# Optimization experiments

Measured on AMD Instinct MI355X. Metric: run time of the kernel, lower is better.

Reference implementation:

```python
import jax, jax.numpy as jnp
import numpy as np

N = 100000
E = 1_600_000
IN = 128
HID = 32
HEADS = 4
OUT = 2
NEG_SLOPE = 0.2  # PyG GATv2Conv default negative_slope


def setup_inputs() -> dict:
    key = jax.random.key(0)
    ks = jax.random.split(key, 18)
    g = lambda k, shape, fan: jax.random.normal(k, shape, dtype=jnp.float32) / np.sqrt(fan)
    return {
        "x": jax.random.normal(ks[0], (N, IN), dtype=jnp.float32),
        "edge_index": jax.random.randint(ks[1], (2, E), 0, N, dtype=jnp.int32),
        # conv1: GATv2Conv(IN, HID, heads=HEADS)
        "W1l": g(ks[2], (IN, HEADS * HID), IN),
        "b1l": jnp.zeros((HEADS * HID,), jnp.float32),
        "W1r": g(ks[3], (IN, HEADS * HID), IN),
        "b1r": jnp.zeros((HEADS * HID,), jnp.float32),
        "att1": g(ks[4], (HEADS, HID), HID),
        "bias1": jnp.zeros((HEADS * HID,), jnp.float32),
        # conv2: GATv2Conv(HEADS*HID, HID, heads=1)
        "W2l": g(ks[5], (HEADS * HID, HID), HEADS * HID),
        "b2l": jnp.zeros((HID,), jnp.float32),
        "W2r": g(ks[6], (HEADS * HID, HID), HEADS * HID),
        "b2r": jnp.zeros((HID,), jnp.float32),
        "att2": g(ks[7], (1, HID), HID),
        "bias2": jnp.zeros((HID,), jnp.float32),
        # final linear
        "Wlin": g(ks[8], (HID, OUT), HID),
        "blin": jnp.zeros((OUT,), jnp.float32),
    }


def _gatv2(x, src, dst, Wl, bl, Wr, br, att, bias, heads, ch):
    n = x.shape[0]
    xl = (x @ Wl + bl).reshape(n, heads, ch)  # source transform
    xr = (x @ Wr + br).reshape(n, heads, ch)  # target transform
    # GATv2 edge score: a^T LeakyReLU(xl_j + xr_i)
    e = jax.nn.leaky_relu(xl[src] + xr[dst], NEG_SLOPE)      # [E, H, C]
    score = jnp.einsum('ehc,hc->eh', e, att)                  # [E, H]
    # segment softmax over edges sharing a destination node
    m = jax.ops.segment_max(score, dst, num_segments=n)
    ex = jnp.exp(score - m[dst])
    denom = jax.ops.segment_sum(ex, dst, num_segments=n)
    alpha = ex / denom[dst]                                   # [E, H]
    out = jax.ops.segment_sum(alpha[..., None] * xl[src], dst, num_segments=n)
    return out.reshape(n, heads * ch) + bias


def reference(x, edge_index, W1l, b1l, W1r, b1r, att1, bias1,
              W2l, b2l, W2r, b2r, att2, bias2, Wlin, blin):
    # add self-loops (PyG GATv2Conv default add_self_loops=True)
    loop = jnp.arange(N, dtype=edge_index.dtype)
    src = jnp.concatenate([edge_index[0], loop])
    dst = jnp.concatenate([edge_index[1], loop])

    h = _gatv2(x, src, dst, W1l, b1l, W1r, b1r, att1, bias1, HEADS, HID)
    h = jax.nn.elu(h)
    # dropout is inactive in eval mode
    h = _gatv2(h, src, dst, W2l, b2l, W2r, b2r, att2, bias2, 1, HID)
    h = jax.nn.elu(h)
    return h @ Wlin + blin  # [N, OUT]
```

## Files before the change

kernel.cpp:

```cpp
#include <hip/hip_runtime.h>
#include <hip/hip_fp16.h>
#include <math.h>

#define N_NODES 100000
#define E_EDGES 1600000
#define ETOT (E_EDGES + N_NODES)
#define NEG 0.2f
#define NB 782
#define BCAP 2560
#define CHUNK 8192
#define NCHB ((ETOT + CHUNK - 1) / CHUNK)

typedef _Float16 half8 __attribute__((ext_vector_type(8)));
typedef _Float16 half4v __attribute__((ext_vector_type(4)));
typedef _Float16 half2v __attribute__((ext_vector_type(2)));
typedef float floatx4 __attribute__((ext_vector_type(4)));

union H8 {
  half8 v;
  _Float16 e[8];
};

__device__ __forceinline__ float elu(float v) { return v > 0.f ? v : (__expf(v) - 1.f); }

__device__ __forceinline__ float score8(half8 a, half8 r, half8 av) {
  half8 t = a + r;
  t = __builtin_elementwise_max(t, t * (_Float16)NEG);
  half8 s8 = t * av;
  half4v s4 = __builtin_shufflevector(s8, s8, 0, 1, 2, 3) +
              __builtin_shufflevector(s8, s8, 4, 5, 6, 7);
  half2v s2 = __builtin_shufflevector(s4, s4, 0, 1) +
              __builtin_shufflevector(s4, s4, 2, 3);
  return (float)s2[0] + (float)s2[1];
}

__global__ __launch_bounds__(256) void bin_kernel(const int* __restrict__ ei,
                                                  unsigned* __restrict__ cursor,
                                                  unsigned* __restrict__ bins) {
  __shared__ unsigned cnt[NB];
  __shared__ unsigned base[NB];
  int t = threadIdx.x;
  for (int b = t; b < NB; b += 256) cnt[b] = 0;
  __syncthreads();
  int e0 = blockIdx.x * CHUNK;
#pragma unroll
  for (int i = 0; i < CHUNK / 256; i++) {
    int e = e0 + i * 256 + t;
    if (e < ETOT) {
      int dst = (e < E_EDGES) ? ei[E_EDGES + e] : (e - E_EDGES);
      atomicAdd(&cnt[dst >> 7], 1u);
    }
  }
  __syncthreads();
  for (int b = t; b < NB; b += 256) {
    unsigned c = cnt[b];
    base[b] = c ? atomicAdd(&cursor[b], c) : 0u;
    cnt[b] = 0;
  }
  __syncthreads();
#pragma unroll
  for (int i = 0; i < CHUNK / 256; i++) {
    int e = e0 + i * 256 + t;
    if (e < ETOT) {
      int src, dst;
      if (e < E_EDGES) { src = ei[e]; dst = ei[E_EDGES + e]; }
      else { src = e - E_EDGES; dst = src; }
      int b = dst >> 7;
      unsigned off = atomicAdd(&cnt[b], 1u);
      bins[(size_t)b * BCAP + base[b] + off] =
          ((unsigned)(dst & 127) << 17) | (unsigned)src;
    }
  }
}

__global__ __launch_bounds__(1024) void scan_buckets(const unsigned* __restrict__ cursor,
                                                     unsigned* __restrict__ bucket_base,
                                                     unsigned* __restrict__ rowptr) {
  __shared__ unsigned s[1024];
  int t = threadIdx.x;
  unsigned v = (t < NB) ? cursor[t] : 0u;
  s[t] = v;
  __syncthreads();
  for (int off = 1; off < 1024; off <<= 1) {
    unsigned a = (t >= off) ? s[t - off] : 0u;
    __syncthreads();
    s[t] += a;
    __syncthreads();
  }
  if (t < NB) bucket_base[t] = s[t] - v;
  if (t == 0) { bucket_base[NB] = ETOT; rowptr[N_NODES] = ETOT; }
}

__global__ __launch_bounds__(256) void scatter2_kernel(const unsigned* __restrict__ bins,
                                                       const unsigned* __restrict__ cursor,
                                                       const unsigned* __restrict__ bucket_base,
                                                       unsigned* __restrict__ rowptr,
                                                       int* __restrict__ csr_src) {
  __shared__ unsigned cnt[128];
  __shared__ unsigned pref[128];
  int b = blockIdx.x, t = threadIdx.x;
  unsigned cntb = cursor[b];
  unsigned bbase = bucket_base[b];
  const unsigned* bp = bins + (size_t)b * BCAP;
  if (t < 128) cnt[t] = 0;
  __syncthreads();
  for (unsigned i = t; i < cntb; i += 256) atomicAdd(&cnt[bp[i] >> 17], 1u);
  __syncthreads();
  if (t < 128) pref[t] = cnt[t];
  __syncthreads();
  for (int off = 1; off < 128; off <<= 1) {
    unsigned a = (t >= off && t < 128) ? pref[t - off] : 0u;
    __syncthreads();
    if (t < 128) pref[t] += a;
    __syncthreads();
  }
  if (t < 128) {
    unsigned excl = pref[t] - cnt[t];
    pref[t] = excl;
    int n = (b << 7) + t;
    if (n < N_NODES) rowptr[n] = bbase + excl;
    cnt[t] = 0;
  }
  __syncthreads();
  for (unsigned i = t; i < cntb; i += 256) {
    unsigned en = bp[i];
    int j = (int)(en >> 17);
    unsigned off = atomicAdd(&cnt[j], 1u);
    csr_src[bbase + pref[j] + off] = (int)(en & 0x1FFFFu);
  }
}

__global__ __launch_bounds__(256) void pack_w_kernel(
    const float* __restrict__ W1l, const float* __restrict__ W1r,
    const float* __restrict__ b1l, const float* __restrict__ b1r,
    const float* __restrict__ W2l, const float* __restrict__ W2r,
    const float* __restrict__ b2l, const float* __restrict__ b2r,
    const float* __restrict__ att1, const float* __restrict__ att2,
    _Float16* __restrict__ Bperm, _Float16* __restrict__ B2perm,
    float* __restrict__ biascat, float* __restrict__ bias2cat,
    _Float16* __restrict__ att1h, _Float16* __restrict__ att2h) {
  int gt = blockIdx.x * 256 + threadIdx.x;
  int gstr = gridDim.x * 256;
  for (int e = gt; e < 4096; e += gstr) {
    int nt = e >> 8, kt = (e >> 6) & 3, lane = e & 63;
    int n = nt * 16 + (lane & 15);
    int kb = kt * 32 + (lane >> 4) * 8;
#pragma unroll
    for (int j = 0; j < 8; j++) {
      int k = kb + j;
      float val = (n < 128) ? W1l[k * 128 + n] : W1r[k * 128 + (n - 128)];
      Bperm[(size_t)e * 8 + j] = (_Float16)val;
    }
  }
  for (int e = gt; e < 1024; e += gstr) {
    int nt = e >> 8, kt = (e >> 6) & 3, lane = e & 63;
    int n = nt * 16 + (lane & 15);
    int kb = kt * 32 + (lane >> 4) * 8;
#pragma unroll
    for (int j = 0; j < 8; j++) {
      int k = kb + j;
      float val = (n < 32) ? W2l[k * 32 + n] : W2r[k * 32 + (n - 32)];
      B2perm[(size_t)e * 8 + j] = (_Float16)val;
    }
  }
  if (blockIdx.x == 0) {
    int t = threadIdx.x;
    biascat[t] = (t < 128) ? b1l[t] : b1r[t - 128];
    if (t < 64) bias2cat[t] = (t < 32) ? b2l[t] : b2r[t - 32];
    if (t < 128) att1h[t] = (_Float16)att1[t];
    if (t < 32) att2h[t] = (_Float16)att2[t];
  }
}

__global__ __launch_bounds__(256) void gemm1_mfma(
    const float* __restrict__ x, const _Float16* __restrict__ Bperm,
    const float* __restrict__ biascat,
    __half* __restrict__ xlh, __half* __restrict__ xrh) {
  __shared__ __align__(16) char smem[64 * 256];
  int t = threadIdx.x;
  int base = blockIdx.x * 64;
  {
    int row = t >> 2, c4 = t & 3;
    int grow = base + row;
    const float* gp = x + (size_t)grow * 128 + c4 * 32;
#pragma unroll
    for (int j = 0; j < 4; j++) {
      half8 v = {};
      if (grow < N_NODES) {
        float4 f0 = *(const float4*)(gp + j * 8);
        float4 f1 = *(const float4*)(gp + j * 8 + 4);
        v[0] = (_Float16)f0.x; v[1] = (_Float16)f0.y;
        v[2] = (_Float16)f0.z; v[3] = (_Float16)f0.w;
        v[4] = (_Float16)f1.x; v[5] = (_Float16)f1.y;
        v[6] = (_Float16)f1.z; v[7] = (_Float16)f1.w;
      }
      int off = row * 256 + ((((c4 * 4 + j) * 16)) ^ ((row & 7) << 4));
      *(half8*)(smem + off) = v;
    }
  }
  int wid = t >> 6, lane = t & 63;
  half8 bf[4][4];
#pragma unroll
  for (int ntl = 0; ntl < 4; ntl++)
#pragma unroll
    for (int kt = 0; kt < 4; kt++) {
      int f = (wid * 4 + ntl) * 4 + kt;
      bf[ntl][kt] = *(const half8*)(Bperm + ((size_t)f * 64 + lane) * 8);
    }
  floatx4 acc[4][4] = {};
  __syncthreads();
#pragma unroll
  for (int kt = 0; kt < 4; kt++) {
    half8 a[4];
#pragma unroll
    for (int mt = 0; mt < 4; mt++) {
      int row = mt * 16 + (lane & 15);
      int kchunk = kt * 4 + (lane >> 4);
      int off = row * 256 + ((kchunk * 16) ^ ((row & 7) << 4));
      a[mt] = *(const half8*)(smem + off);
    }
#pragma unroll
    for (int mt = 0; mt < 4; mt++)
#pragma unroll
      for (int ntl = 0; ntl < 4; ntl++)
        acc[mt][ntl] = __builtin_amdgcn_mfma_f32_16x16x32_f16(a[mt], bf[ntl][kt],
                                                              acc[mt][ntl], 0, 0, 0);
  }
#pragma unroll
  for (int mt = 0; mt < 4; mt++) {
#pragma unroll
    for (int i = 0; i < 4; i++) {
      int row = base + mt * 16 + (lane >> 4) * 4 + i;
      if (row >= N_NODES) continue;
#pragma unroll
      for (int ntl = 0; ntl < 4; ntl++) {
        int col = wid * 64 + ntl * 16 + (lane & 15);
        float v = acc[mt][ntl][i] + biascat[col];
        if (col < 128) xlh[(size_t)row * 128 + col] = __float2half_rn(v);
        else xrh[(size_t)row * 128 + (col - 128)] = __float2half_rn(v);
      }
    }
  }
}

__global__ __launch_bounds__(256) void gemm2_mfma(
    const __half* __restrict__ h1h, const _Float16* __restrict__ B2perm,
    const float* __restrict__ bias2cat,
    __half* __restrict__ xl2h, __half* __restrict__ xr2h) {
  __shared__ __align__(16) char smem[64 * 256];
  int t = threadIdx.x;
  int base = blockIdx.x * 64;
  {
    int row = t >> 2, c4 = t & 3;
    int grow = base + row;
    const char* gp = (const char*)(h1h + (size_t)grow * 128 + c4 * 32);
#pragma unroll
    for (int j = 0; j < 4; j++) {
      half8 v = {};
      if (grow < N_NODES) v = *(const half8*)(gp + j * 16);
      int off = row * 256 + ((((c4 * 4 + j) * 16)) ^ ((row & 7) << 4));
      *(half8*)(smem + off) = v;
    }
  }
  int wid = t >> 6, lane = t & 63;
  half8 bf[4];
#pragma unroll
  for (int kt = 0; kt < 4; kt++) {
    int f = wid * 4 + kt;
    bf[kt] = *(const half8*)(B2perm + ((size_t)f * 64 + lane) * 8);
  }
  floatx4 acc[4] = {};
  __syncthreads();
#pragma unroll
  for (int kt = 0; kt < 4; kt++) {
    half8 a[4];
#pragma unroll
    for (int mt = 0; mt < 4; mt++) {
      int row = mt * 16 + (lane & 15);
      int kchunk = kt * 4 + (lane >> 4);
      int off = row * 256 + ((kchunk * 16) ^ ((row & 7) << 4));
      a[mt] = *(const half8*)(smem + off);
    }
#pragma unroll
    for (int mt = 0; mt < 4; mt++)
      acc[mt] = __builtin_amdgcn_mfma_f32_16x16x32_f16(a[mt], bf[kt], acc[mt], 0, 0, 0);
  }
  int col = wid * 16 + (lane & 15);
  float bv = bias2cat[col];
#pragma unroll
  for (int mt = 0; mt < 4; mt++) {
#pragma unroll
    for (int i = 0; i < 4; i++) {
      int row = base + mt * 16 + (lane >> 4) * 4 + i;
      if (row >= N_NODES) continue;
      float v = acc[mt][i] + bv;
      if (col < 32) xl2h[(size_t)row * 32 + col] = __float2half_rn(v);
      else xr2h[(size_t)row * 32 + (col - 32)] = __float2half_rn(v);
    }
  }
}

__global__ __launch_bounds__(256) void l1_gather_kernel(
    const __half* __restrict__ xlh, const __half* __restrict__ xrh,
    const int* __restrict__ csr_src, const unsigned* __restrict__ rowptr,
    const _Float16* __restrict__ att1h, const float* __restrict__ bias,
    __half* __restrict__ h1h) {
  int wid = threadIdx.x >> 6;
  int lane = threadIdx.x & 63;
  int n = blockIdx.x * 4 + wid;
  if (n >= N_NODES) return;
  int g = lane >> 4;
  int q = lane & 15;
  int c0 = q * 8;
  half8 rv = *(const half8*)(xrh + (size_t)n * 128 + c0);
  half8 av = *(const half8*)(att1h + c0);
  unsigned beg = rowptr[n], end = rowptr[n + 1];
  int nit = (int)(end - beg + 3) >> 2;
  float d = 0.f;
  float acc[8] = {0.f};
  for (int i = 0; i < nit; i++) {
    unsigned e = beg + i * 4 + g;
    bool valid = e < end;
    int s = csr_src[valid ? e : (end - 1)];
    H8 a;
    a.v = *(const half8*)(xlh + (size_t)s * 128 + c0);
    float v = score8(a.v, rv, av);
    v += __shfl_xor(v, 1);
    v += __shfl_xor(v, 2);
    float p = valid ? __expf(v) : 0.f;
    d += p;
#pragma unroll
    for (int j = 0; j < 8; j++) acc[j] = fmaf(p, (float)a.e[j], acc[j]);
  }
#pragma unroll
  for (int msk = 16; msk <= 32; msk <<= 1) {
    d += __shfl_xor(d, msk);
#pragma unroll
    for (int j = 0; j < 8; j++) acc[j] += __shfl_xor(acc[j], msk);
  }
  if (g == 0) {
    float inv = 1.f / d;
    H8 res;
#pragma unroll
    for (int j = 0; j < 8; j++)
      res.e[j] = (_Float16)elu(acc[j] * inv + bias[c0 + j]);
    *(half8*)(h1h + (size_t)n * 128 + c0) = res.v;
  }
}

__global__ __launch_bounds__(256) void l2_gather_kernel(
    const __half* __restrict__ xl2h, const __half* __restrict__ xr2h,
    const int* __restrict__ csr_src, const unsigned* __restrict__ rowptr,
    const _Float16* __restrict__ att2h, const float* __restrict__ bias,
    const float* __restrict__ Wlin, const float* __restrict__ blin,
    float* __restrict__ out) {
  int wid = threadIdx.x >> 6;
  int lane = threadIdx.x & 63;
  int n = blockIdx.x * 4 + wid;
  if (n >= N_NODES) return;
  int g = lane >> 2;
  int q = lane & 3;
  int c0 = q * 8;
  half8 rv = *(const half8*)(xr2h + (size_t)n * 32 + c0);
  half8 av = *(const half8*)(att2h + c0);
  unsigned beg = rowptr[n], end = rowptr[n + 1];
  int nit = (int)(end - beg + 15) >> 4;
  float d = 0.f;
  float acc[8] = {0.f};
  for (int i = 0; i < nit; i++) {
    unsigned e = beg + i * 16 + g;
    bool valid = e < end;
    int s = csr_src[valid ? e : (end - 1)];
    H8 a;
    a.v = *(const half8*)(xl2h + (size_t)s * 32 + c0);
    float v = score8(a.v, rv, av);
    v += __shfl_xor(v, 1);
    v += __shfl_xor(v, 2);
    float p = valid ? __expf(v) : 0.f;
    d += p;
#pragma unroll
    for (int j = 0; j < 8; j++) acc[j] = fmaf(p, (float)a.e[j], acc[j]);
  }
#pragma unroll
  for (int msk = 4; msk <= 32; msk <<= 1) {
    d += __shfl_xor(d, msk);
#pragma unroll
    for (int j = 0; j < 8; j++) acc[j] += __shfl_xor(acc[j], msk);
  }
  float inv = 1.f / d;
  float o0 = 0.f, o1 = 0.f;
#pragma unroll
  for (int j = 0; j < 8; j++) {
    float v = elu(acc[j] * inv + bias[c0 + j]);
    o0 = fmaf(v, Wlin[(c0 + j) * 2 + 0], o0);
    o1 = fmaf(v, Wlin[(c0 + j) * 2 + 1], o1);
  }
  o0 += __shfl_xor(o0, 1); o1 += __shfl_xor(o1, 1);
  o0 += __shfl_xor(o0, 2); o1 += __shfl_xor(o1, 2);
  if (lane == 0) {
    out[(size_t)n * 2 + 0] = o0 + blin[0];
    out[(size_t)n * 2 + 1] = o1 + blin[1];
  }
}

extern "C" void kernel_launch(void* const* d_in, const int* in_sizes, int n_in,
                              void* d_out, int out_size, void* d_ws, size_t ws_size,
                              hipStream_t stream) {
  const float* x     = (const float*)d_in[0];
  const int*   ei    = (const int*)d_in[1];
  const float* W1l   = (const float*)d_in[2];
  const float* b1l   = (const float*)d_in[3];
  const float* W1r   = (const float*)d_in[4];
  const float* b1r   = (const float*)d_in[5];
  const float* att1  = (const float*)d_in[6];
  const float* bias1 = (const float*)d_in[7];
  const float* W2l   = (const float*)d_in[8];
  const float* b2l   = (const float*)d_in[9];
  const float* W2r   = (const float*)d_in[10];
  const float* b2r   = (const float*)d_in[11];
  const float* att2  = (const float*)d_in[12];
  const float* bias2 = (const float*)d_in[13];
  const float* Wlin  = (const float*)d_in[14];
  const float* blin  = (const float*)d_in[15];
  float* out = (float*)d_out;

  __half* xl1h  = (__half*)d_ws;
  __half* xr1h  = xl1h + (size_t)N_NODES * 128;
  __half* h1h   = xr1h + (size_t)N_NODES * 128;
  __half* xl2h  = h1h + (size_t)N_NODES * 128;
  __half* xr2h  = xl2h + (size_t)N_NODES * 32;
  _Float16* Bperm  = (_Float16*)(xr2h + (size_t)N_NODES * 32);
  _Float16* B2perm = Bperm + 32768;
  _Float16* att1h  = B2perm + 8192;
  _Float16* att2h  = att1h + 128;
  float* biascat   = (float*)(att2h + 32);
  float* bias2cat  = biascat + 256;
  int* csr_src     = (int*)(bias2cat + 64);
  unsigned* rowptr = (unsigned*)(csr_src + (size_t)ETOT);
  unsigned* cursor = rowptr + (N_NODES + 1);
  unsigned* bucket_base = cursor + NB;
  unsigned* bins   = bucket_base + NB + 1;

  pack_w_kernel<<<20, 256, 0, stream>>>(W1l, W1r, b1l, b1r, W2l, W2r, b2l, b2r,
                                        att1, att2, Bperm, B2perm, biascat, bias2cat,
                                        att1h, att2h);

  (void)hipMemsetAsync(cursor, 0, (size_t)NB * sizeof(unsigned), stream);
  bin_kernel<<<NCHB, 256, 0, stream>>>(ei, cursor, bins);
  scan_buckets<<<1, 1024, 0, stream>>>(cursor, bucket_base, rowptr);
  scatter2_kernel<<<NB, 256, 0, stream>>>(bins, cursor, bucket_base, rowptr, csr_src);

  gemm1_mfma<<<(N_NODES + 63) / 64, 256, 0, stream>>>(x, Bperm, biascat, xl1h, xr1h);
  l1_gather_kernel<<<(N_NODES + 3) / 4, 256, 0, stream>>>(
      (const __half*)xl1h, (const __half*)xr1h, csr_src, rowptr, att1h, bias1, h1h);

  gemm2_mfma<<<(N_NODES + 63) / 64, 256, 0, stream>>>(h1h, B2perm, bias2cat, xl2h, xr2h);
  l2_gather_kernel<<<(N_NODES + 3) / 4, 256, 0, stream>>>(
      xl2h, xr2h, csr_src, rowptr, att2h, bias2, Wlin, blin, out);
}
```

Measured before the change: 266.6 us.

## Fuse independent kernels by block range and accumulate gathers in half precision

```diff
diff --git a/kernel.cpp b/kernel.cpp
--- a/kernel.cpp
+++ b/kernel.cpp
@@ -10,15 +10,17 @@
 #define BCAP 2560
 #define CHUNK 8192
 #define NCHB ((ETOT + CHUNK - 1) / CHUNK)
+#define GEMM1_BLOCKS ((N_NODES + 63) / 64)
 
 typedef _Float16 half8 __attribute__((ext_vector_type(8)));
 typedef _Float16 half4v __attribute__((ext_vector_type(4)));
 typedef _Float16 half2v __attribute__((ext_vector_type(2)));
 typedef float floatx4 __attribute__((ext_vector_type(4)));
 
-union H8 {
+union H8I {
   half8 v;
   _Float16 e[8];
+  int i[4];
 };
 
 __device__ __forceinline__ float elu(float v) { return v > 0.f ? v : (__expf(v) - 1.f); }
@@ -34,41 +36,85 @@
   return (float)s2[0] + (float)s2[1];
 }
 
-__global__ __launch_bounds__(256) void bin_kernel(const int* __restrict__ ei,
-                                                  unsigned* __restrict__ cursor,
-                                                  unsigned* __restrict__ bins) {
-  __shared__ unsigned cnt[NB];
-  __shared__ unsigned base[NB];
+__global__ __launch_bounds__(256) void fusedA_kernel(
+    const int* __restrict__ ei, unsigned* __restrict__ cursor,
+    unsigned* __restrict__ bins,
+    const float* __restrict__ W1l, const float* __restrict__ W1r,
+    const float* __restrict__ b1l, const float* __restrict__ b1r,
+    const float* __restrict__ W2l, const float* __restrict__ W2r,
+    const float* __restrict__ b2l, const float* __restrict__ b2r,
+    const float* __restrict__ att1, const float* __restrict__ att2,
+    _Float16* __restrict__ Bperm, _Float16* __restrict__ B2perm,
+    float* __restrict__ biascat, float* __restrict__ bias2cat,
+    _Float16* __restrict__ att1h, _Float16* __restrict__ att2h) {
   int t = threadIdx.x;
-  for (int b = t; b < NB; b += 256) cnt[b] = 0;
-  __syncthreads();
-  int e0 = blockIdx.x * CHUNK;
-#pragma unroll
-  for (int i = 0; i < CHUNK / 256; i++) {
-    int e = e0 + i * 256 + t;
-    if (e < ETOT) {
-      int dst = (e < E_EDGES) ? ei[E_EDGES + e] : (e - E_EDGES);
-      atomicAdd(&cnt[dst >> 7], 1u);
-    }
-  }
-  __syncthreads();
-  for (int b = t; b < NB; b += 256) {
-    unsigned c = cnt[b];
-    base[b] = c ? atomicAdd(&cursor[b], c) : 0u;
-    cnt[b] = 0;
-  }
-  __syncthreads();
-#pragma unroll
-  for (int i = 0; i < CHUNK / 256; i++) {
-    int e = e0 + i * 256 + t;
-    if (e < ETOT) {
-      int src, dst;
-      if (e < E_EDGES) { src = ei[e]; dst = ei[E_EDGES + e]; }
-      else { src = e - E_EDGES; dst = src; }
-      int b = dst >> 7;
-      unsigned off = atomicAdd(&cnt[b], 1u);
-      bins[(size_t)b * BCAP + base[b] + off] =
-          ((unsigned)(dst & 127) << 17) | (unsigned)src;
+  if (blockIdx.x < NCHB) {
+    __shared__ unsigned cnt[NB];
+    __shared__ unsigned base[NB];
+    for (int b = t; b < NB; b += 256) cnt[b] = 0;
+    __syncthreads();
+    int e0 = blockIdx.x * CHUNK;
+    int dstr[CHUNK / 256];
+#pragma unroll
+    for (int i = 0; i < CHUNK / 256; i++) {
+      int e = e0 + i * 256 + t;
+      int dst = 0;
+      if (e < ETOT) {
+        dst = (e < E_EDGES) ? ei[E_EDGES + e] : (e - E_EDGES);
+        atomicAdd(&cnt[dst >> 7], 1u);
+      }
+      dstr[i] = dst;
+    }
+    __syncthreads();
+    for (int b = t; b < NB; b += 256) {
+      unsigned c = cnt[b];
+      base[b] = c ? atomicAdd(&cursor[b], c) : 0u;
+      cnt[b] = 0;
+    }
+    __syncthreads();
+#pragma unroll
+    for (int i = 0; i < CHUNK / 256; i++) {
+      int e = e0 + i * 256 + t;
+      if (e < ETOT) {
+        int dst = dstr[i];
+        int src = (e < E_EDGES) ? ei[e] : dst;
+        int b = dst >> 7;
+        unsigned off = atomicAdd(&cnt[b], 1u);
+        bins[(size_t)b * BCAP + base[b] + off] =
+            ((unsigned)(dst & 127) << 17) | (unsigned)src;
+      }
+    }
+  } else {
+    int pb = blockIdx.x - NCHB;
+    int gt = pb * 256 + t;
+    int gstr = 20 * 256;
+    for (int e = gt; e < 4096; e += gstr) {
+      int nt = e >> 8, kt = (e >> 6) & 3, lane = e & 63;
+      int n = nt * 16 + (lane & 15);
+      int kb = kt * 32 + (lane >> 4) * 8;
+#pragma unroll
+      for (int j = 0; j < 8; j++) {
+        int k = kb + j;
+        float val = (n < 128) ? W1l[k * 128 + n] : W1r[k * 128 + (n - 128)];
+        Bperm[(size_t)e * 8 + j] = (_Float16)val;
+      }
+    }
+    for (int e = gt; e < 1024; e += gstr) {
+      int nt = e >> 8, kt = (e >> 6) & 3, lane = e & 63;
+      int n = nt * 16 + (lane & 15);
+      int kb = kt * 32 + (lane >> 4) * 8;
+#pragma unroll
+      for (int j = 0; j < 8; j++) {
+        int k = kb + j;
+        float val = (n < 32) ? W2l[k * 32 + n] : W2r[k * 32 + (n - 32)];
+        B2perm[(size_t)e * 8 + j] = (_Float16)val;
+      }
+    }
+    if (pb == 0) {
+      biascat[t] = (t < 128) ? b1l[t] : b1r[t - 128];
+      if (t < 64) bias2cat[t] = (t < 32) ? b2l[t] : b2r[t - 32];
+      if (t < 128) att1h[t] = (_Float16)att1[t];
+      if (t < 32) att2h[t] = (_Float16)att2[t];
     }
   }
 }
@@ -91,153 +137,110 @@
   if (t == 0) { bucket_base[NB] = ETOT; rowptr[N_NODES] = ETOT; }
 }
 
-__global__ __launch_bounds__(256) void scatter2_kernel(const unsigned* __restrict__ bins,
-                                                       const unsigned* __restrict__ cursor,
-                                                       const unsigned* __restrict__ bucket_base,
-                                                       unsigned* __restrict__ rowptr,
-                                                       int* __restrict__ csr_src) {
-  __shared__ unsigned cnt[128];
-  __shared__ unsigned pref[128];
-  int b = blockIdx.x, t = threadIdx.x;
-  unsigned cntb = cursor[b];
-  unsigned bbase = bucket_base[b];
-  const unsigned* bp = bins + (size_t)b * BCAP;
-  if (t < 128) cnt[t] = 0;
-  __syncthreads();
-  for (unsigned i = t; i < cntb; i += 256) atomicAdd(&cnt[bp[i] >> 17], 1u);
-  __syncthreads();
-  if (t < 128) pref[t] = cnt[t];
-  __syncthreads();
-  for (int off = 1; off < 128; off <<= 1) {
-    unsigned a = (t >= off && t < 128) ? pref[t - off] : 0u;
-    __syncthreads();
-    if (t < 128) pref[t] += a;
-    __syncthreads();
-  }
-  if (t < 128) {
-    unsigned excl = pref[t] - cnt[t];
-    pref[t] = excl;
-    int n = (b << 7) + t;
-    if (n < N_NODES) rowptr[n] = bbase + excl;
-    cnt[t] = 0;
-  }
-  __syncthreads();
-  for (unsigned i = t; i < cntb; i += 256) {
-    unsigned en = bp[i];
-    int j = (int)(en >> 17);
-    unsigned off = atomicAdd(&cnt[j], 1u);
-    csr_src[bbase + pref[j] + off] = (int)(en & 0x1FFFFu);
-  }
-}
-
-__global__ __launch_bounds__(256) void pack_w_kernel(
-    const float* __restrict__ W1l, const float* __restrict__ W1r,
-    const float* __restrict__ b1l, const float* __restrict__ b1r,
-    const float* __restrict__ W2l, const float* __restrict__ W2r,
-    const float* __restrict__ b2l, const float* __restrict__ b2r,
-    const float* __restrict__ att1, const float* __restrict__ att2,
-    _Float16* __restrict__ Bperm, _Float16* __restrict__ B2perm,
-    float* __restrict__ biascat, float* __restrict__ bias2cat,
-    _Float16* __restrict__ att1h, _Float16* __restrict__ att2h) {
-  int gt = blockIdx.x * 256 + threadIdx.x;
-  int gstr = gridDim.x * 256;
-  for (int e = gt; e < 4096; e += gstr) {
-    int nt = e >> 8, kt = (e >> 6) & 3, lane = e & 63;
-    int n = nt * 16 + (lane & 15);
-    int kb = kt * 32 + (lane >> 4) * 8;
-#pragma unroll
-    for (int j = 0; j < 8; j++) {
-      int k = kb + j;
-      float val = (n < 128) ? W1l[k * 128 + n] : W1r[k * 128 + (n - 128)];
-      Bperm[(size_t)e * 8 + j] = (_Float16)val;
-    }
-  }
-  for (int e = gt; e < 1024; e += gstr) {
-    int nt = e >> 8, kt = (e >> 6) & 3, lane = e & 63;
-    int n = nt * 16 + (lane & 15);
-    int kb = kt * 32 + (lane >> 4) * 8;
-#pragma unroll
-    for (int j = 0; j < 8; j++) {
-      int k = kb + j;
-      float val = (n < 32) ? W2l[k * 32 + n] : W2r[k * 32 + (n - 32)];
-      B2perm[(size_t)e * 8 + j] = (_Float16)val;
-    }
-  }
-  if (blockIdx.x == 0) {
-    int t = threadIdx.x;
-    biascat[t] = (t < 128) ? b1l[t] : b1r[t - 128];
-    if (t < 64) bias2cat[t] = (t < 32) ? b2l[t] : b2r[t - 32];
-    if (t < 128) att1h[t] = (_Float16)att1[t];
-    if (t < 32) att2h[t] = (_Float16)att2[t];
-  }
-}
-
-__global__ __launch_bounds__(256) void gemm1_mfma(
+__global__ __launch_bounds__(256) void fusedB_kernel(
+    const unsigned* __restrict__ bins, const unsigned* __restrict__ cursor,
+    const unsigned* __restrict__ bucket_base,
+    unsigned* __restrict__ rowptr, int* __restrict__ csr_src,
     const float* __restrict__ x, const _Float16* __restrict__ Bperm,
     const float* __restrict__ biascat,
     __half* __restrict__ xlh, __half* __restrict__ xrh) {
   __shared__ __align__(16) char smem[64 * 256];
   int t = threadIdx.x;
-  int base = blockIdx.x * 64;
-  {
-    int row = t >> 2, c4 = t & 3;
-    int grow = base + row;
-    const float* gp = x + (size_t)grow * 128 + c4 * 32;
-#pragma unroll
-    for (int j = 0; j < 4; j++) {
-      half8 v = {};
-      if (grow < N_NODES) {
-        float4 f0 = *(const float4*)(gp + j * 8);
-        float4 f1 = *(const float4*)(gp + j * 8 + 4);
-        v[0] = (_Float16)f0.x; v[1] = (_Float16)f0.y;
-        v[2] = (_Float16)f0.z; v[3] = (_Float16)f0.w;
-        v[4] = (_Float16)f1.x; v[5] = (_Float16)f1.y;
-        v[6] = (_Float16)f1.z; v[7] = (_Float16)f1.w;
-      }
-      int off = row * 256 + ((((c4 * 4 + j) * 16)) ^ ((row & 7) << 4));
-      *(half8*)(smem + off) = v;
-    }
-  }
-  int wid = t >> 6, lane = t & 63;
-  half8 bf[4][4];
-#pragma unroll
-  for (int ntl = 0; ntl < 4; ntl++)
+  if (blockIdx.x < NB) {
+    unsigned* cnt = (unsigned*)smem;
+    unsigned* pref = cnt + 128;
+    int b = blockIdx.x;
+    unsigned cntb = cursor[b];
+    unsigned bbase = bucket_base[b];
+    const unsigned* bp = bins + (size_t)b * BCAP;
+    if (t < 128) cnt[t] = 0;
+    __syncthreads();
+    for (unsigned i = t; i < cntb; i += 256) atomicAdd(&cnt[bp[i] >> 17], 1u);
+    __syncthreads();
+    if (t < 128) pref[t] = cnt[t];
+    __syncthreads();
+    for (int off = 1; off < 128; off <<= 1) {
+      unsigned a = (t >= off && t < 128) ? pref[t - off] : 0u;
+      __syncthreads();
+      if (t < 128) pref[t] += a;
+      __syncthreads();
+    }
+    if (t < 128) {
+      unsigned excl = pref[t] - cnt[t];
+      pref[t] = excl;
+      int n = (b << 7) + t;
+      if (n < N_NODES) rowptr[n] = bbase + excl;
+      cnt[t] = 0;
+    }
+    __syncthreads();
+    for (unsigned i = t; i < cntb; i += 256) {
+      unsigned en = bp[i];
+      int j = (int)(en >> 17);
+      unsigned off = atomicAdd(&cnt[j], 1u);
+      csr_src[bbase + pref[j] + off] = (int)(en & 0x1FFFFu);
+    }
+  } else {
+    int base = (blockIdx.x - NB) * 64;
+    {
+      int row = t >> 2, c4 = t & 3;
+      int grow = base + row;
+      const float* gp = x + (size_t)grow * 128 + c4 * 32;
+#pragma unroll
+      for (int j = 0; j < 4; j++) {
+        half8 v = {};
+        if (grow < N_NODES) {
+          float4 f0 = *(const float4*)(gp + j * 8);
+          float4 f1 = *(const float4*)(gp + j * 8 + 4);
+          v[0] = (_Float16)f0.x; v[1] = (_Float16)f0.y;
+          v[2] = (_Float16)f0.z; v[3] = (_Float16)f0.w;
+          v[4] = (_Float16)f1.x; v[5] = (_Float16)f1.y;
+          v[6] = (_Float16)f1.z; v[7] = (_Float16)f1.w;
+        }
+        int off = row * 256 + ((((c4 * 4 + j) * 16)) ^ ((row & 7) << 4));
+        *(half8*)(smem + off) = v;
+      }
+    }
+    int wid = t >> 6, lane = t & 63;
+    half8 bf[4][4];
+#pragma unroll
+    for (int ntl = 0; ntl < 4; ntl++)
+#pragma unroll
+      for (int kt = 0; kt < 4; kt++) {
+        int f = (wid * 4 + ntl) * 4 + kt;
+        bf[ntl][kt] = *(const half8*)(Bperm + ((size_t)f * 64 + lane) * 8);
+      }
+    floatx4 acc[4][4] = {};
+    __syncthreads();
 #pragma unroll
     for (int kt = 0; kt < 4; kt++) {
-      int f = (wid * 4 + ntl) * 4 + kt;
-      bf[ntl][kt] = *(const half8*)(Bperm + ((size_t)f * 64 + lane) * 8);
-    }
-  floatx4 acc[4][4] = {};
-  __syncthreads();
-#pragma unroll
-  for (int kt = 0; kt < 4; kt++) {
-    half8 a[4];
+      half8 a[4];
+#pragma unroll
+      for (int mt = 0; mt < 4; mt++) {
+        int row = mt * 16 + (lane & 15);
+        int kchunk = kt * 4 + (lane >> 4);
+        int off = row * 256 + ((kchunk * 16) ^ ((row & 7) << 4));
+        a[mt] = *(const half8*)(smem + off);
+      }
+#pragma unroll
+      for (int mt = 0; mt < 4; mt++)
+#pragma unroll
+        for (int ntl = 0; ntl < 4; ntl++)
+          acc[mt][ntl] = __builtin_amdgcn_mfma_f32_16x16x32_f16(a[mt], bf[ntl][kt],
+                                                                acc[mt][ntl], 0, 0, 0);
+    }
 #pragma unroll
     for (int mt = 0; mt < 4; mt++) {
-      int row = mt * 16 + (lane & 15);
-      int kchunk = kt * 4 + (lane >> 4);
-      int off = row * 256 + ((kchunk * 16) ^ ((row & 7) << 4));
-      a[mt] = *(const half8*)(smem + off);
-    }
-#pragma unroll
-    for (int mt = 0; mt < 4; mt++)
-#pragma unroll
-      for (int ntl = 0; ntl < 4; ntl++)
-        acc[mt][ntl] = __builtin_amdgcn_mfma_f32_16x16x32_f16(a[mt], bf[ntl][kt],
-                                                              acc[mt][ntl], 0, 0, 0);
-  }
-#pragma unroll
-  for (int mt = 0; mt < 4; mt++) {
-#pragma unroll
-    for (int i = 0; i < 4; i++) {
-      int row = base + mt * 16 + (lane >> 4) * 4 + i;
-      if (row >= N_NODES) continue;
-#pragma unroll
-      for (int ntl = 0; ntl < 4; ntl++) {
-        int col = wid * 64 + ntl * 16 + (lane & 15);
-        float v = acc[mt][ntl][i] + biascat[col];
-        if (col < 128) xlh[(size_t)row * 128 + col] = __float2half_rn(v);
-        else xrh[(size_t)row * 128 + (col - 128)] = __float2half_rn(v);
+#pragma unroll
+      for (int i = 0; i < 4; i++) {
+        int row = base + mt * 16 + (lane >> 4) * 4 + i;
+        if (row >= N_NODES) continue;
+#pragma unroll
+        for (int ntl = 0; ntl < 4; ntl++) {
+          int col = wid * 64 + ntl * 16 + (lane & 15);
+          float v = acc[mt][ntl][i] + biascat[col];
+          if (col < 128) xlh[(size_t)row * 128 + col] = __float2half_rn(v);
+          else xrh[(size_t)row * 128 + (col - 128)] = __float2half_rn(v);
+        }
       }
     }
   }
@@ -317,33 +320,37 @@
   unsigned beg = rowptr[n], end = rowptr[n + 1];
   int nit = (int)(end - beg + 3) >> 2;
   float d = 0.f;
-  float acc[8] = {0.f};
+  H8I acc;
+  acc.v = (half8){};
   for (int i = 0; i < nit; i++) {
     unsigned e = beg + i * 4 + g;
     bool valid = e < end;
     int s = csr_src[valid ? e : (end - 1)];
-    H8 a;
+    H8I a;
     a.v = *(const half8*)(xlh + (size_t)s * 128 + c0);
     float v = score8(a.v, rv, av);
     v += __shfl_xor(v, 1);
     v += __shfl_xor(v, 2);
-    float p = valid ? __expf(v) : 0.f;
+    float p = valid ? __expf(v - 4.f) : 0.f;
     d += p;
-#pragma unroll
-    for (int j = 0; j < 8; j++) acc[j] = fmaf(p, (float)a.e[j], acc[j]);
+    _Float16 ph = (_Float16)p;
+    half8 p8 = {ph, ph, ph, ph, ph, ph, ph, ph};
+    acc.v = p8 * a.v + acc.v;
   }
 #pragma unroll
   for (int msk = 16; msk <= 32; msk <<= 1) {
     d += __shfl_xor(d, msk);
-#pragma unroll
-    for (int j = 0; j < 8; j++) acc[j] += __shfl_xor(acc[j], msk);
+    H8I o;
+#pragma unroll
+    for (int k = 0; k < 4; k++) o.i[k] = __shfl_xor(acc.i[k], msk);
+    acc.v = acc.v + o.v;
   }
   if (g == 0) {
     float inv = 1.f / d;
-    H8 res;
+    H8I res;
 #pragma unroll
     for (int j = 0; j < 8; j++)
-      res.e[j] = (_Float16)elu(acc[j] * inv + bias[c0 + j]);
+      res.e[j] = (_Float16)elu((float)acc.e[j] * inv + bias[c0 + j]);
     *(half8*)(h1h + (size_t)n * 128 + c0) = res.v;
   }
 }
@@ -366,32 +373,36 @@
   unsigned beg = rowptr[n], end = rowptr[n + 1];
   int nit = (int)(end - beg + 15) >> 4;
   float d = 0.f;
-  float acc[8] = {0.f};
+  H8I acc;
+  acc.v = (half8){};
   for (int i = 0; i < nit; i++) {
     unsigned e = beg + i * 16 + g;
     bool valid = e < end;
     int s = csr_src[valid ? e : (end - 1)];
-    H8 a;
+    H8I a;
     a.v = *(const half8*)(xl2h + (size_t)s * 32 + c0);
     float v = score8(a.v, rv, av);
     v += __shfl_xor(v, 1);
     v += __shfl_xor(v, 2);
-    float p = valid ? __expf(v) : 0.f;
+    float p = valid ? __expf(v - 4.f) : 0.f;
     d += p;
-#pragma unroll
-    for (int j = 0; j < 8; j++) acc[j] = fmaf(p, (float)a.e[j], acc[j]);
+    _Float16 ph = (_Float16)p;
+    half8 p8 = {ph, ph, ph, ph, ph, ph, ph, ph};
+    acc.v = p8 * a.v + acc.v;
   }
 #pragma unroll
   for (int msk = 4; msk <= 32; msk <<= 1) {
     d += __shfl_xor(d, msk);
-#pragma unroll
-    for (int j = 0; j < 8; j++) acc[j] += __shfl_xor(acc[j], msk);
+    H8I o;
+#pragma unroll
+    for (int k = 0; k < 4; k++) o.i[k] = __shfl_xor(acc.i[k], msk);
+    acc.v = acc.v + o.v;
   }
   float inv = 1.f / d;
   float o0 = 0.f, o1 = 0.f;
 #pragma unroll
   for (int j = 0; j < 8; j++) {
-    float v = elu(acc[j] * inv + bias[c0 + j]);
+    float v = elu((float)acc.e[j] * inv + bias[c0 + j]);
     o0 = fmaf(v, Wlin[(c0 + j) * 2 + 0], o0);
     o1 = fmaf(v, Wlin[(c0 + j) * 2 + 1], o1);
   }
@@ -441,20 +452,18 @@
   unsigned* bucket_base = cursor + NB;
   unsigned* bins   = bucket_base + NB + 1;
 
-  pack_w_kernel<<<20, 256, 0, stream>>>(W1l, W1r, b1l, b1r, W2l, W2r, b2l, b2r,
-                                        att1, att2, Bperm, B2perm, biascat, bias2cat,
-                                        att1h, att2h);
-
   (void)hipMemsetAsync(cursor, 0, (size_t)NB * sizeof(unsigned), stream);
-  bin_kernel<<<NCHB, 256, 0, stream>>>(ei, cursor, bins);
+  fusedA_kernel<<<NCHB + 20, 256, 0, stream>>>(
+      ei, cursor, bins, W1l, W1r, b1l, b1r, W2l, W2r, b2l, b2r, att1, att2,
+      Bperm, B2perm, biascat, bias2cat, att1h, att2h);
   scan_buckets<<<1, 1024, 0, stream>>>(cursor, bucket_base, rowptr);
-  scatter2_kernel<<<NB, 256, 0, stream>>>(bins, cursor, bucket_base, rowptr, csr_src);
-
-  gemm1_mfma<<<(N_NODES + 63) / 64, 256, 0, stream>>>(x, Bperm, biascat, xl1h, xr1h);
+  fusedB_kernel<<<NB + GEMM1_BLOCKS, 256, 0, stream>>>(
+      bins, cursor, bucket_base, rowptr, csr_src, x, Bperm, biascat, xl1h, xr1h);
+
   l1_gather_kernel<<<(N_NODES + 3) / 4, 256, 0, stream>>>(
       (const __half*)xl1h, (const __half*)xr1h, csr_src, rowptr, att1h, bias1, h1h);
 
-  gemm2_mfma<<<(N_NODES + 63) / 64, 256, 0, stream>>>(h1h, B2perm, bias2cat, xl2h, xr2h);
+  gemm2_mfma<<<GEMM1_BLOCKS, 256, 0, stream>>>(h1h, B2perm, bias2cat, xl2h, xr2h);
   l2_gather_kernel<<<(N_NODES + 3) / 4, 256, 0, stream>>>(
       xl2h, xr2h, csr_src, rowptr, att2h, bias2, Wlin, blin, out);
 }
```

Result: faster. 251.5 us (-5.7%).
